# Performance work log

Measured on AMD Instinct MI355X. Metric: run time of the kernel, lower is better.

Reference implementation:

```python
import jax, jax.numpy as jnp
import numpy as np

N = 100000          # nodes
F_IN = 500          # num_features
HID = 256           # hidden
C = 40              # out_classes
E = 2302585         # ~ N*ln(N)*ec, doubled (both directions) in spar_samp
ALPHA0 = 0.1        # att[0][0] = alpha*(1-alpha)**0


def setup_inputs() -> dict:
    key = jax.random.key(0)
    ks = jax.random.split(key, 8)
    x = jax.random.normal(ks[0], (N, F_IN), dtype=jnp.float32)
    W1 = jax.random.normal(ks[1], (F_IN, HID), dtype=jnp.float32) * (1.0 / np.sqrt(F_IN))
    b1 = jnp.zeros((HID,), dtype=jnp.float32)
    W2 = jax.random.normal(ks[2], (HID, C), dtype=jnp.float32) * (1.0 / np.sqrt(HID))
    b2 = jnp.zeros((C,), dtype=jnp.float32)
    edge_row = jax.random.randint(ks[3], (E,), 0, N, dtype=jnp.int64) if jax.config.jax_enable_x64 else jax.random.randint(ks[3], (E,), 0, N, dtype=jnp.int32)
    edge_col = jax.random.randint(ks[4], (E,), 0, N, dtype=edge_row.dtype)
    # sampled importance weights: deg^{-1/2}*deg^{-1/2}*(M/num_edgess) -> small positive floats
    edge_val = jax.random.uniform(ks[5], (E,), dtype=jnp.float32, minval=0.001, maxval=0.05)
    return {"x": x, "W1": W1, "b1": b1, "W2": W2, "b2": b2,
            "edge_row": edge_row, "edge_col": edge_col, "edge_val": edge_val}


def reference(x, W1, b1, W2, b2, edge_row, edge_col, edge_val):
    # eval mode: dropout is identity
    h = jax.nn.relu(x @ W1 + b1)          # [N, HID]
    h = h @ W2 + b2                       # [N, C]
    # sparse propagation: out[r] += val * h[c]  (scatter-add SpMM)
    msg = edge_val[:, None] * h[edge_col]            # [E, C] gather
    agg = jax.ops.segment_sum(msg, edge_row, num_segments=N)  # [N, C]
    out = h * ALPHA0 + agg
    return jax.nn.log_softmax(out, axis=1)
```

## Files before the change

kernel.cpp:

```cpp
#include <hip/hip_runtime.h>
#include <hip/hip_bf16.h>


#define N_NODES 100000
#define F_IN    500
#define HID     256
#define C_OUT   40
#define ALPHA0  0.1f
#define H2STRIDE 64

#define RPB     64
#define NBUCK   ((N_NODES + RPB - 1) / RPB)
#define NBUCKP  1568
#define NCH     1024
#define SCAN_M  (NBUCK * NCH)
#define SCAN_CHUNK 2048
#define NBS     ((SCAN_M + SCAN_CHUNK - 1) / SCAN_CHUNK)
#define BCAPL   1792

typedef short short8 __attribute__((ext_vector_type(8)));
typedef float f32x4  __attribute__((ext_vector_type(4)));

__device__ __forceinline__ short f2bf(float f) {
  union { float f; unsigned u; } x; x.f = f;
  unsigned r = x.u + 0x7fffu + ((x.u >> 16) & 1u);
  return (short)(r >> 16);
}
__device__ __forceinline__ float bf2f(short s) {
  union { unsigned u; float f; } x; x.u = ((unsigned)(unsigned short)s) << 16;
  return x.f;
}
__device__ __forceinline__ unsigned cvtpk(float lo, float hi) {
  unsigned r;
  asm("v_cvt_pk_bf16_f32 %0, %1, %2" : "=v"(r) : "v"(lo), "v"(hi));
  return r;
}
__device__ __forceinline__ void lbar() {
  asm volatile("s_waitcnt lgkmcnt(0)" ::: "memory");
  __builtin_amdgcn_s_barrier();
}
__device__ __forceinline__ void gll16(const float* g, const char* l) {
  __builtin_amdgcn_global_load_lds(
      (const __attribute__((address_space(1))) void*)g,
      (__attribute__((address_space(3))) void*)l, 16, 0, 0);
}

__global__ __launch_bounds__(256) void k_pack_weights(
    const float* __restrict__ W1, const float* __restrict__ W2,
    short* __restrict__ W1S, short* __restrict__ W2T)
{
  int i = blockIdx.x * 256 + threadIdx.x;
  if (i < 16*256*32) {
    int kc  = i >> 13;
    int idx = i & 8191;
    int n   = idx >> 5;
    int kk  = idx & 31;
    int k   = kc*32 + kk;
    float v = (k < F_IN) ? W1[k*HID + n] : 0.f;
    W1S[i] = f2bf(v);
  } else {
    int j = i - 16*256*32;
    if (j < 48*256) {
      int n = j >> 8;
      int k = j & 255;
      float v = (n < C_OUT) ? W2[k*C_OUT + n] : 0.f;
      W2T[j] = f2bf(v);
    }
  }
}

__global__ __launch_bounds__(512, 4) void k_fused_mlp(
    const float* __restrict__ x, const float* __restrict__ b1v,
    const float* __restrict__ b2v,
    const short* __restrict__ W1S, const short* __restrict__ W2T,
    short* __restrict__ h2b,
    const int* __restrict__ erow, int* __restrict__ hs, int E, int CH)
{
  __shared__ __align__(16) char smem[65536];
  short (*Hl)[256] = (short(*)[256])smem;

  const int tid  = threadIdx.x;
  const int w    = tid >> 6;
  const int lane = tid & 63;
  const int lr   = lane & 15;
  const int quad = lane >> 4;
  const int wr   = w >> 2;
  const int wc   = w & 3;
  const int row0 = blockIdx.x * 128;

  const int s_rl0 = (w*2)*8 + (lane>>3);
  const int s_rl1 = (w*2+1)*8 + (lane>>3);
  const int ksw   = ((lane&7) ^ ((lane>>3)&7)) * 4;
  const float* gp0 = x + (size_t)min(row0 + s_rl0, N_NODES-1) * F_IN;
  const float* gp1 = x + (size_t)min(row0 + s_rl1, N_NODES-1) * F_IN;
  const char* l0 = smem + (w*2)*1024;
  const char* l1 = smem + (w*2+1)*1024;

  f32x4 acc[4][4] = {};

  #pragma unroll
  for (int p = 0; p < 2; ++p) {
    int kb = p*32 + ksw;
    const float* a0 = (kb + 4 <= F_IN) ? gp0 + kb : x;
    const float* a1 = (kb + 4 <= F_IN) ? gp1 + kb : x;
    gll16(a0, l0 + p*16384);
    gll16(a1, l1 + p*16384);
  }

  const short* bbase = W1S + (wc*64 + lr)*32 + quad*8;
  const int m2 = lr & 7;

  #pragma unroll
  for (int kc = 0; kc < 16; ++kc) {
    short8 bf4[4];
    #pragma unroll
    for (int t = 0; t < 4; ++t)
      bf4[t] = *(const short8*)(bbase + kc*8192 + t*16*32);
    __builtin_amdgcn_sched_barrier(0);

    if (kc < 14) {
      int kb = (kc+2)*32 + ksw;
      const float* a0 = (kb + 4 <= F_IN) ? gp0 + kb : x;
      const float* a1 = (kb + 4 <= F_IN) ? gp1 + kb : x;
      gll16(a0, l0 + ((kc+2)&3)*16384);
      gll16(a1, l1 + ((kc+2)&3)*16384);
      __builtin_amdgcn_sched_barrier(0);
      asm volatile("s_waitcnt vmcnt(8)" ::: "memory");
    } else if (kc == 14) {
      asm volatile("s_waitcnt vmcnt(6)" ::: "memory");
    } else {
      asm volatile("s_waitcnt vmcnt(4)" ::: "memory");
    }
    __builtin_amdgcn_s_barrier();

    const char* Abase = smem + (kc & 3)*16384;
    short8 af[4];
    #pragma unroll
    for (int t = 0; t < 4; ++t) {
      int rl = wr*64 + t*16 + lr;
      f32x4 u0 = *(const f32x4*)(Abase + rl*128 + (((quad*2  ) ^ m2) << 4));
      f32x4 u1 = *(const f32x4*)(Abase + rl*128 + (((quad*2+1) ^ m2) << 4));
      union { unsigned u[4]; short8 s; } pk;
      pk.u[0] = cvtpk(u0[0], u0[1]);
      pk.u[1] = cvtpk(u0[2], u0[3]);
      pk.u[2] = cvtpk(u1[0], u1[1]);
      pk.u[3] = cvtpk(u1[2], u1[3]);
      af[t] = pk.s;
    }

    #pragma unroll
    for (int rt = 0; rt < 4; ++rt)
      #pragma unroll
      for (int ct = 0; ct < 4; ++ct)
        acc[rt][ct] = __builtin_amdgcn_mfma_f32_16x16x32_bf16(af[rt], bf4[ct], acc[rt][ct], 0, 0, 0);
  }
  lbar();

  #pragma unroll
  for (int ct = 0; ct < 4; ++ct) {
    int col = wc*64 + ct*16 + lr;
    int cg = col >> 3, ci = col & 7;
    float bias = b1v[col];
    #pragma unroll
    for (int rt = 0; rt < 4; ++rt) {
      #pragma unroll
      for (int r = 0; r < 4; ++r) {
        int row = wr*64 + rt*16 + quad*4 + r;
        float v = fmaxf(acc[rt][ct][r] + bias, 0.f);
        Hl[row][((cg ^ (row & 31)) << 3) | ci] = f2bf(v);
      }
    }
  }
  lbar();

  f32x4 acc2[3] = {};
  const int arow = w*16 + lr;
  #pragma unroll
  for (int kc2 = 0; kc2 < 8; ++kc2) {
    int gg = kc2*4 + quad;
    short8 a2 = *(const short8*)&Hl[arow][(gg ^ (arow & 31)) << 3];
    #pragma unroll
    for (int nt = 0; nt < 3; ++nt) {
      short8 b2 = *(const short8*)(W2T + (nt*16 + lr)*256 + kc2*32 + quad*8);
      acc2[nt] = __builtin_amdgcn_mfma_f32_16x16x32_bf16(a2, b2, acc2[nt], 0, 0, 0);
    }
  }

  #pragma unroll
  for (int nt = 0; nt < 3; ++nt) {
    int col = nt*16 + lr;
    float bias = (col < C_OUT) ? b2v[col] : 0.f;
    #pragma unroll
    for (int r = 0; r < 4; ++r) {
      int row = row0 + w*16 + quad*4 + r;
      if (row < N_NODES) {
        float v = (col < C_OUT) ? (acc2[nt][r] + bias) : 0.f;
        h2b[(long)row * H2STRIDE + col] = f2bf(v);
      }
    }
  }
  {
    int col = 48 + lr;
    #pragma unroll
    for (int r = 0; r < 4; ++r) {
      int row = row0 + w*16 + quad*4 + r;
      if (row < N_NODES) h2b[(long)row * H2STRIDE + col] = 0;
    }
  }

  int* hcnt = (int*)smem;
  for (int cc = blockIdx.x; cc < NCH; cc += gridDim.x) {
    lbar();
    for (int b = tid; b < NBUCK; b += 512) hcnt[b] = 0;
    __syncthreads();
    int e0 = cc * CH, e1 = min(E, e0 + CH);
    if (e0 < e1) {
      int g0 = e0 >> 2, g1 = e1 >> 2;
      const int4* rp = (const int4*)erow;
      for (int g = g0 + tid; g < g1; g += 512) {
        int4 r4 = rp[g];
        atomicAdd(&hcnt[r4.x >> 6], 1);
        atomicAdd(&hcnt[r4.y >> 6], 1);
        atomicAdd(&hcnt[r4.z >> 6], 1);
        atomicAdd(&hcnt[r4.w >> 6], 1);
      }
      for (int e = (g1 << 2) + tid; e < e1; e += 512)
        atomicAdd(&hcnt[erow[e] >> 6], 1);
    }
    __syncthreads();
    for (int b = tid; b < NBUCK; b += 512)
      hs[(size_t)cc * NBUCKP + b] = hcnt[b];
  }
}

__global__ __launch_bounds__(256) void k_transpose(
    const int* __restrict__ hs, int* __restrict__ offs)
{
  __shared__ int t[64][65];
  int cb = blockIdx.x & 15;
  int bb = blockIdx.x >> 4;
  int c0 = cb * 64, b0 = bb * 64;
  int j  = threadIdx.x & 63;
  int i0 = threadIdx.x >> 6;
  #pragma unroll
  for (int k = 0; k < 16; ++k) {
    int i = i0 + k * 4;
    int b = b0 + j;
    t[i][j] = (b < NBUCK) ? hs[(size_t)(c0 + i) * NBUCKP + b] : 0;
  }
  __syncthreads();
  #pragma unroll
  for (int k = 0; k < 16; ++k) {
    int i = i0 + k * 4;
    int b = b0 + i;
    if (b < NBUCK) offs[(size_t)b * NCH + c0 + j] = t[j][i];
  }
}

__global__ __launch_bounds__(256) void k_scan1(
    int* __restrict__ offs, int* __restrict__ bsums)
{
  __shared__ int sh[256];
  int tid = threadIdx.x;
  int base = blockIdx.x * SCAN_CHUNK + tid * 8;
  int d[8];
  #pragma unroll
  for (int k = 0; k < 8; ++k)
    d[k] = (base + k < SCAN_M) ? offs[base + k] : 0;
  int s = 0;
  #pragma unroll
  for (int k = 0; k < 8; ++k) s += d[k];
  sh[tid] = s;
  __syncthreads();
  for (int o = 1; o < 256; o <<= 1) {
    int v = (tid >= o) ? sh[tid - o] : 0;
    __syncthreads();
    if (tid >= o) sh[tid] += v;
    __syncthreads();
  }
  int run = sh[tid] - s;
  #pragma unroll
  for (int k = 0; k < 8; ++k) {
    if (base + k < SCAN_M) offs[base + k] = run;
    run += d[k];
  }
  if (tid == 255) bsums[blockIdx.x] = sh[255];
}

__global__ __launch_bounds__(256) void k_scan2(int* __restrict__ bsums) {
  __shared__ int sh[256];
  int tid = threadIdx.x;
  int d[4];
  int s = 0;
  #pragma unroll
  for (int k = 0; k < 4; ++k) {
    int i = tid * 4 + k;
    d[k] = (i < NBS) ? bsums[i] : 0;
    s += d[k];
  }
  sh[tid] = s;
  __syncthreads();
  for (int o = 1; o < 256; o <<= 1) {
    int u = (tid >= o) ? sh[tid - o] : 0;
    __syncthreads();
    if (tid >= o) sh[tid] += u;
    __syncthreads();
  }
  int run = sh[tid] - s;
  #pragma unroll
  for (int k = 0; k < 4; ++k) {
    int i = tid * 4 + k;
    if (i < NBS) bsums[i] = run;
    run += d[k];
  }
}

__global__ __launch_bounds__(256) void k_split(
    const int* __restrict__ erow, const int* __restrict__ ecol,
    const float* __restrict__ eval, const int* __restrict__ offs,
    const int* __restrict__ bsums, int2* __restrict__ sorted,
    int* __restrict__ bstart, int E, int CH)
{
  __shared__ int cur[NBUCK];
  int tid = threadIdx.x, c = blockIdx.x;

  for (int b = tid; b < NBUCK; b += 256) {
    int m = b * NCH + c;
    int val = offs[m] + bsums[m >> 11];
    cur[b] = val;
    if (c == 0) bstart[b] = val;
  }
  if (c == 0 && tid == 0) bstart[NBUCK] = E;
  __syncthreads();

  int e0 = c * CH, e1 = min(E, e0 + CH);
  if (e0 >= e1) return;
  int g0 = e0 >> 2, g1 = e1 >> 2;
  const int4*   rp = (const int4*)erow;
  const int4*   cp = (const int4*)ecol;
  const float4* vp = (const float4*)eval;
  for (int g = g0 + tid; g < g1; g += 256) {
    int4 r4 = rp[g];
    int4 c4 = cp[g];
    float4 v4 = vp[g];
    int p0 = atomicAdd(&cur[r4.x >> 6], 1);
    int p1 = atomicAdd(&cur[r4.y >> 6], 1);
    int p2 = atomicAdd(&cur[r4.z >> 6], 1);
    int p3 = atomicAdd(&cur[r4.w >> 6], 1);
    int2 cv;
    cv.x = c4.x | ((r4.x & 63) << 17); cv.y = __float_as_int(v4.x); sorted[p0] = cv;
    cv.x = c4.y | ((r4.y & 63) << 17); cv.y = __float_as_int(v4.y); sorted[p1] = cv;
    cv.x = c4.z | ((r4.z & 63) << 17); cv.y = __float_as_int(v4.z); sorted[p2] = cv;
    cv.x = c4.w | ((r4.w & 63) << 17); cv.y = __float_as_int(v4.w); sorted[p3] = cv;
  }
  for (int e = (g1 << 2) + tid; e < e1; e += 256) {
    int r = erow[e];
    int pos = atomicAdd(&cur[r >> 6], 1);
    int2 cv;
    cv.x = ecol[e] | ((r & 63) << 17);
    cv.y = __float_as_int(eval[e]);
    sorted[pos] = cv;
  }
}

__global__ __launch_bounds__(256) void k_csr_spmm(
    const int* __restrict__ bstart, const int2* __restrict__ sorted,
    const short* __restrict__ h2b, float* __restrict__ out)
{
  __shared__ int2 eS[BCAPL];
  __shared__ int h[RPB];
  __shared__ int roff[RPB];
  __shared__ int cur[RPB];
  int tid = threadIdx.x, b = blockIdx.x;
  int lane = tid & 63, w = tid >> 6;
  int start = bstart[b], end = bstart[b + 1];
  int cnt = end - start;

  int2 cv[7];
  int nloc = 0;
  for (int i = tid, k = 0; i < cnt; i += 256, ++k) { cv[k] = sorted[start + i]; nloc = k + 1; }

  if (tid < RPB) h[tid] = 0;
  __syncthreads();
  for (int k = 0; k < nloc; ++k)
    atomicAdd(&h[((unsigned)cv[k].x) >> 17], 1);
  __syncthreads();
  if (tid < RPB) roff[tid] = h[tid];
  __syncthreads();
  for (int o = 1; o < RPB; o <<= 1) {
    int u = (tid >= o && tid < RPB) ? roff[tid - o] : 0;
    __syncthreads();
    if (tid >= o && tid < RPB) roff[tid] += u;
    __syncthreads();
  }
  if (tid < RPB) cur[tid] = roff[tid] - h[tid];
  __syncthreads();
  for (int k = 0; k < nloc; ++k) {
    unsigned rl = ((unsigned)cv[k].x) >> 17;
    int p = atomicAdd(&cur[rl], 1);
    if (p < BCAPL) eS[p] = cv[k];
  }
  __syncthreads();

  for (int rr = 0; rr < 16; ++rr) {
    int r = w * 16 + rr;
    int row = b * RPB + r;
    if (row >= N_NODES) continue;
    float acc = ALPHA0 * bf2f(h2b[(size_t)row * H2STRIDE + lane]);
    int e  = roff[r] - h[r];
    int ee = roff[r];
    for (; e + 7 < ee; e += 8) {
      int2 cc[8];
      float gg[8];
      #pragma unroll
      for (int j = 0; j < 8; ++j) cc[j] = eS[e + j];
      #pragma unroll
      for (int j = 0; j < 8; ++j)
        gg[j] = bf2f(h2b[(size_t)(cc[j].x & 0x1FFFF) * H2STRIDE + lane]);
      #pragma unroll
      for (int j = 0; j < 8; ++j) acc += __int_as_float(cc[j].y) * gg[j];
    }
    for (; e + 3 < ee; e += 4) {
      int2 c0 = eS[e], c1 = eS[e+1], c2 = eS[e+2], c3 = eS[e+3];
      float g0 = bf2f(h2b[(size_t)(c0.x & 0x1FFFF) * H2STRIDE + lane]);
      float g1 = bf2f(h2b[(size_t)(c1.x & 0x1FFFF) * H2STRIDE + lane]);
      float g2 = bf2f(h2b[(size_t)(c2.x & 0x1FFFF) * H2STRIDE + lane]);
      float g3 = bf2f(h2b[(size_t)(c3.x & 0x1FFFF) * H2STRIDE + lane]);
      acc += __int_as_float(c0.y) * g0;
      acc += __int_as_float(c1.y) * g1;
      acc += __int_as_float(c2.y) * g2;
      acc += __int_as_float(c3.y) * g3;
    }
    for (; e < ee; ++e) {
      int2 c0 = eS[e];
      acc += __int_as_float(c0.y) * bf2f(h2b[(size_t)(c0.x & 0x1FFFF) * H2STRIDE + lane]);
    }
    float m = (lane < C_OUT) ? acc : -INFINITY;
    #pragma unroll
    for (int o = 32; o > 0; o >>= 1) m = fmaxf(m, __shfl_xor(m, o));
    float ev = (lane < C_OUT) ? __expf(acc - m) : 0.f;
    float s = ev;
    #pragma unroll
    for (int o = 32; o > 0; o >>= 1) s += __shfl_xor(s, o);
    if (lane < C_OUT) out[(long)row * C_OUT + lane] = acc - m - __logf(s);
  }
}

extern "C" void kernel_launch(void* const* d_in, const int* in_sizes, int n_in,
                              void* d_out, int out_size, void* d_ws, size_t ws_size,
                              hipStream_t stream) {
  const float* x    = (const float*)d_in[0];
  const float* W1   = (const float*)d_in[1];
  const float* b1   = (const float*)d_in[2];
  const float* W2   = (const float*)d_in[3];
  const float* b2   = (const float*)d_in[4];
  const int*   erow = (const int*)d_in[5];
  const int*   ecol = (const int*)d_in[6];
  const float* eval = (const float*)d_in[7];
  const int E  = in_sizes[5];
  int CH = (E + NCH - 1) / NCH;
  CH = (CH + 3) & ~3;

  char* p = (char*)d_ws;
  short* h2b    = (short*)p;  p += (size_t)N_NODES * H2STRIDE * 2;
  short* W1S    = (short*)p;  p += (size_t)16*256*32 * 2;
  short* W2T    = (short*)p;  p += (size_t)48*256 * 2;
  int*   hs     = (int*)p;    p += (size_t)NCH * NBUCKP * 4;
  int*   offs   = (int*)p;    p += (size_t)SCAN_M * 4;
  int*   bsums  = (int*)p;    p += 1024 * 4;
  int*   bstart = (int*)p;    p += (size_t)(NBUCK + 4) * 4;
  int2*  sorted = (int2*)p;
  float* out = (float*)d_out;

  k_pack_weights<<<(16*256*32 + 48*256 + 255)/256, 256, 0, stream>>>(W1, W2, W1S, W2T);
  k_fused_mlp<<<(N_NODES + 127)/128, 512, 0, stream>>>(x, b1, b2, W1S, W2T, h2b,
                                                       erow, hs, E, CH);
  k_transpose<<<16 * 25, 256, 0, stream>>>(hs, offs);
  k_scan1<<<NBS, 256, 0, stream>>>(offs, bsums);
  k_scan2<<<1, 256, 0, stream>>>(bsums);
  k_split<<<NCH, 256, 0, stream>>>(erow, ecol, eval, offs, bsums, sorted, bstart, E, CH);
  k_csr_spmm<<<NBUCK, 256, 0, stream>>>(bstart, sorted, h2b, out);
}
```

Before: 502.3 us.

## Cut histogram chunk count to 256 and rework split and bucket-local sort

Reduces the number of edge chunks used for the bucket histogram from 1024 to 256. This shrinks the histogram matrix, the transpose, the scan and the scan2 work, and the split kernel is widened to 512 threads per block to cover larger chunks. In the SpMM kernel, the per-thread register staging of edges is replaced by two passes that reread the sorted edges from global memory, and the 64-entry row prefix sum now uses a wavefront shuffle scan instead of a barrier-based shared-memory scan. The tradeoff is fewer blocks in the histogram and split phases, so less parallelism and more atomic contention per block, plus a second global read of each bucket's edges.

```diff
diff --git a/kernel.cpp b/kernel.cpp
--- a/kernel.cpp
+++ b/kernel.cpp
@@ -12,7 +12,7 @@
 #define RPB     64
 #define NBUCK   ((N_NODES + RPB - 1) / RPB)
 #define NBUCKP  1568
-#define NCH     1024
+#define NCH     256
 #define SCAN_M  (NBUCK * NCH)
 #define SCAN_CHUNK 2048
 #define NBS     ((SCAN_M + SCAN_CHUNK - 1) / SCAN_CHUNK)
@@ -208,8 +208,9 @@
     }
   }
 
-  int* hcnt = (int*)smem;
-  for (int cc = blockIdx.x; cc < NCH; cc += gridDim.x) {
+  if (blockIdx.x < NCH) {
+    int cc = blockIdx.x;
+    int* hcnt = (int*)smem;
     lbar();
     for (int b = tid; b < NBUCK; b += 512) hcnt[b] = 0;
     __syncthreads();
@@ -237,8 +238,8 @@
     const int* __restrict__ hs, int* __restrict__ offs)
 {
   __shared__ int t[64][65];
-  int cb = blockIdx.x & 15;
-  int bb = blockIdx.x >> 4;
+  int cb = blockIdx.x & 3;
+  int bb = blockIdx.x >> 2;
   int c0 = cb * 64, b0 = bb * 64;
   int j  = threadIdx.x & 63;
   int i0 = threadIdx.x >> 6;
@@ -290,15 +291,8 @@
 __global__ __launch_bounds__(256) void k_scan2(int* __restrict__ bsums) {
   __shared__ int sh[256];
   int tid = threadIdx.x;
-  int d[4];
-  int s = 0;
-  #pragma unroll
-  for (int k = 0; k < 4; ++k) {
-    int i = tid * 4 + k;
-    d[k] = (i < NBS) ? bsums[i] : 0;
-    s += d[k];
-  }
-  sh[tid] = s;
+  int v = (tid < NBS) ? bsums[tid] : 0;
+  sh[tid] = v;
   __syncthreads();
   for (int o = 1; o < 256; o <<= 1) {
     int u = (tid >= o) ? sh[tid - o] : 0;
@@ -306,16 +300,10 @@
     if (tid >= o) sh[tid] += u;
     __syncthreads();
   }
-  int run = sh[tid] - s;
-  #pragma unroll
-  for (int k = 0; k < 4; ++k) {
-    int i = tid * 4 + k;
-    if (i < NBS) bsums[i] = run;
-    run += d[k];
-  }
-}
-
-__global__ __launch_bounds__(256) void k_split(
+  if (tid < NBS) bsums[tid] = sh[tid] - v;
+}
+
+__global__ __launch_bounds__(512) void k_split(
     const int* __restrict__ erow, const int* __restrict__ ecol,
     const float* __restrict__ eval, const int* __restrict__ offs,
     const int* __restrict__ bsums, int2* __restrict__ sorted,
@@ -324,7 +312,7 @@
   __shared__ int cur[NBUCK];
   int tid = threadIdx.x, c = blockIdx.x;
 
-  for (int b = tid; b < NBUCK; b += 256) {
+  for (int b = tid; b < NBUCK; b += 512) {
     int m = b * NCH + c;
     int val = offs[m] + bsums[m >> 11];
     cur[b] = val;
@@ -339,7 +327,7 @@
   const int4*   rp = (const int4*)erow;
   const int4*   cp = (const int4*)ecol;
   const float4* vp = (const float4*)eval;
-  for (int g = g0 + tid; g < g1; g += 256) {
+  for (int g = g0 + tid; g < g1; g += 512) {
     int4 r4 = rp[g];
     int4 c4 = cp[g];
     float4 v4 = vp[g];
@@ -353,7 +341,7 @@
     cv.x = c4.z | ((r4.z & 63) << 17); cv.y = __float_as_int(v4.z); sorted[p2] = cv;
     cv.x = c4.w | ((r4.w & 63) << 17); cv.y = __float_as_int(v4.w); sorted[p3] = cv;
   }
-  for (int e = (g1 << 2) + tid; e < e1; e += 256) {
+  for (int e = (g1 << 2) + tid; e < e1; e += 512) {
     int r = erow[e];
     int pos = atomicAdd(&cur[r >> 6], 1);
     int2 cv;
@@ -376,29 +364,27 @@
   int start = bstart[b], end = bstart[b + 1];
   int cnt = end - start;
 
-  int2 cv[7];
-  int nloc = 0;
-  for (int i = tid, k = 0; i < cnt; i += 256, ++k) { cv[k] = sorted[start + i]; nloc = k + 1; }
-
   if (tid < RPB) h[tid] = 0;
   __syncthreads();
-  for (int k = 0; k < nloc; ++k)
-    atomicAdd(&h[((unsigned)cv[k].x) >> 17], 1);
-  __syncthreads();
-  if (tid < RPB) roff[tid] = h[tid];
-  __syncthreads();
-  for (int o = 1; o < RPB; o <<= 1) {
-    int u = (tid >= o && tid < RPB) ? roff[tid - o] : 0;
-    __syncthreads();
-    if (tid >= o && tid < RPB) roff[tid] += u;
-    __syncthreads();
-  }
-  if (tid < RPB) cur[tid] = roff[tid] - h[tid];
-  __syncthreads();
-  for (int k = 0; k < nloc; ++k) {
-    unsigned rl = ((unsigned)cv[k].x) >> 17;
-    int p = atomicAdd(&cur[rl], 1);
-    if (p < BCAPL) eS[p] = cv[k];
+  for (int i = tid; i < cnt; i += 256)
+    atomicAdd(&h[((unsigned)sorted[start + i].x) >> 17], 1);
+  __syncthreads();
+  if (w == 0) {
+    int v = h[lane];
+    int hv = v;
+    #pragma unroll
+    for (int o = 1; o < 64; o <<= 1) {
+      int t = __shfl_up(v, o);
+      if (lane >= o) v += t;
+    }
+    roff[lane] = v;
+    cur[lane]  = v - hv;
+  }
+  __syncthreads();
+  for (int i = tid; i < cnt; i += 256) {
+    int2 cv = sorted[start + i];
+    int p = atomicAdd(&cur[((unsigned)cv.x) >> 17], 1);
+    if (p < BCAPL) eS[p] = cv;
   }
   __syncthreads();
 
@@ -467,7 +453,7 @@
   short* W2T    = (short*)p;  p += (size_t)48*256 * 2;
   int*   hs     = (int*)p;    p += (size_t)NCH * NBUCKP * 4;
   int*   offs   = (int*)p;    p += (size_t)SCAN_M * 4;
-  int*   bsums  = (int*)p;    p += 1024 * 4;
+  int*   bsums  = (int*)p;    p += 256 * 4;
   int*   bstart = (int*)p;    p += (size_t)(NBUCK + 4) * 4;
   int2*  sorted = (int2*)p;
   float* out = (float*)d_out;
@@ -475,9 +461,9 @@
   k_pack_weights<<<(16*256*32 + 48*256 + 255)/256, 256, 0, stream>>>(W1, W2, W1S, W2T);
   k_fused_mlp<<<(N_NODES + 127)/128, 512, 0, stream>>>(x, b1, b2, W1S, W2T, h2b,
                                                        erow, hs, E, CH);
-  k_transpose<<<16 * 25, 256, 0, stream>>>(hs, offs);
+  k_transpose<<<4 * 25, 256, 0, stream>>>(hs, offs);
   k_scan1<<<NBS, 256, 0, stream>>>(offs, bsums);
   k_scan2<<<1, 256, 0, stream>>>(bsums);
-  k_split<<<NCH, 256, 0, stream>>>(erow, ecol, eval, offs, bsums, sorted, bstart, E, CH);
+  k_split<<<NCH, 512, 0, stream>>>(erow, ecol, eval, offs, bsums, sorted, bstart, E, CH);
   k_csr_spmm<<<NBUCK, 256, 0, stream>>>(bstart, sorted, h2b, out);
 }
```

Result: faster. 478.8 us (-4.7%).
